# Kernel optimization log

Measured on AMD Instinct MI355X. Metric: run time of the kernel, lower is better.

Reference implementation:

```python
import jax, jax.numpy as jnp
import numpy as np

QMAX = 127.0

def setup_inputs() -> dict:
    key = jax.random.key(0)
    kx, kw, ks = jax.random.split(key, 3)
    B, S, D_IN, D_OUT = 4, 2048, 4096, 4096
    x = jax.random.normal(kx, (B, S, D_IN), dtype=jnp.float16)
    # int8 weight buffer, same distribution as torch.randint(-127, 127)
    weight = jax.random.randint(kw, (D_OUT, D_IN), -127, 127, dtype=jnp.int32).astype(jnp.int8)
    # per-output-channel weight scales (fp16 buffer); small positive values
    weight_scales = (jax.random.uniform(ks, (D_OUT,), dtype=jnp.float32) * 0.01 + 1e-4).astype(jnp.float16)
    return {"x": x, "weight": weight, "weight_scales": weight_scales}

def reference(x, weight, weight_scales):
    # x: [B, S, D_in] fp16; weight: [D_out, D_in] int8; weight_scales: [D_out] fp16
    x32 = x.astype(jnp.float32)
    # dynamic per-token absmax quantization: scale = absmax / 127
    absmax = jnp.max(jnp.abs(x32), axis=-1, keepdims=True)      # [B, S, 1]
    x_scales = jnp.maximum(absmax / QMAX, 1e-8)
    q = jnp.round(x32 / x_scales)                                # in [-127, 127]
    q = jnp.clip(q, -QMAX, QMAX).astype(jnp.int8)
    # int8 GEMM accumulated in int32 (cupy.matmul on int32 in the original)
    y = jnp.einsum('bsk,nk->bsn', q.astype(jnp.int32), weight.astype(jnp.int32),
                   preferred_element_type=jnp.int32)             # [B, S, D_out]
    # dequant: per-token activation scale * per-channel weight scale
    y = y.astype(jnp.float32) * x_scales * weight_scales.astype(jnp.float32)[None, None, :]
    return y.astype(jnp.float16)
```

## Files before the change

kernel.cpp:

```cpp
#include <hip/hip_runtime.h>
#include <stdint.h>

typedef int int32x4 __attribute__((ext_vector_type(4)));

constexpr int K_DIM = 4096;
constexpr int N_DIM = 4096;
constexpr float QMAXF = 127.0f;

__global__ __launch_bounds__(256) void quant_t(const float* __restrict__ x,
                                               int8_t* __restrict__ qt,
                                               float* __restrict__ scales) {
    __shared__ int8_t lq[16][4112];
    const int b = blockIdx.x;
    const int tid = threadIdx.x;
    const int row16 = tid >> 4;
    const int j = tid & 15;
    const size_t rbase = ((size_t)b * 16 + row16) * K_DIM;
    const float4* xr = reinterpret_cast<const float4*>(x + rbase);

    float m = 0.0f;
#pragma unroll 4
    for (int i = 0; i < 16; ++i) {
        const int c = j + 16 * i;
#pragma unroll
        for (int s = 0; s < 4; ++s) {
            float4 v = xr[c * 4 + s];
            m = fmaxf(m, fmaxf(fmaxf(fabsf(v.x), fabsf(v.y)),
                               fmaxf(fabsf(v.z), fabsf(v.w))));
        }
    }
#pragma unroll
    for (int off = 8; off > 0; off >>= 1) m = fmaxf(m, __shfl_xor(m, off));
    const float scale = fmaxf(m * (1.0f / 127.0f), 1e-8f);
    if (j == 0) scales[b * 16 + row16] = scale;
    const float inv = 1.0f / scale;

#pragma unroll 4
    for (int i = 0; i < 16; ++i) {
        const int c = j + 16 * i;
        int w[4];
#pragma unroll
        for (int s = 0; s < 4; ++s) {
            float4 v = xr[c * 4 + s];
            int b0 = ((int)fminf(QMAXF, fmaxf(-QMAXF, rintf(v.x * inv)))) & 255;
            int b1 = ((int)fminf(QMAXF, fmaxf(-QMAXF, rintf(v.y * inv)))) & 255;
            int b2 = ((int)fminf(QMAXF, fmaxf(-QMAXF, rintf(v.z * inv)))) & 255;
            int b3 = ((int)fminf(QMAXF, fmaxf(-QMAXF, rintf(v.w * inv)))) & 255;
            w[s] = b0 | (b1 << 8) | (b2 << 16) | (b3 << 24);
        }
        *reinterpret_cast<int32x4*>(&lq[row16][c * 16]) = (int32x4){w[0], w[1], w[2], w[3]};
    }
    __syncthreads();

    int8_t* outp = qt + (size_t)b * 65536;
#pragma unroll
    for (int i = 0; i < 16; ++i) {
        const int u = tid + 256 * i;
        int32x4 v = *reinterpret_cast<const int32x4*>(&lq[u & 15][(u >> 4) * 16]);
        *reinterpret_cast<int32x4*>(outp + (size_t)u * 16) = v;
    }
}

__global__ __launch_bounds__(256) void pack_w(const int* __restrict__ w,
                                              int8_t* __restrict__ w8) {
    const int idx = blockIdx.x * 256 + threadIdx.x;
    const int4 v = reinterpret_cast<const int4*>(w)[idx];
    int packed = (v.x & 255) | ((v.y & 255) << 8) | ((v.z & 255) << 16) | ((v.w & 255) << 24);
    reinterpret_cast<int*>(w8)[idx] = packed;
}

constexpr int BM = 256, BN = 256, BKB = 128;
constexpr int NT = K_DIM / BKB;
constexpr int BSLOT = 32768;

#define GLL(src, dst)                                                          \
    __builtin_amdgcn_global_load_lds(                                          \
        (const __attribute__((address_space(1))) unsigned int*)(src),          \
        (__attribute__((address_space(3))) unsigned int*)(dst), 16, 0, 0)

#define MFMA_I8(a, b, c) __builtin_amdgcn_mfma_i32_16x16x64_i8((a), (b), (c), 0, 0, 0)

__global__ __launch_bounds__(512, 2) void w8a8_flat(
        const int8_t* __restrict__ QT, const int8_t* __restrict__ B,
        const float* __restrict__ asc, const float* __restrict__ wsc,
        float* __restrict__ C, int M) {
    extern __shared__ int8_t lds[];

    const int tid  = threadIdx.x;
    const int lane = tid & 63;
    const int wave = tid >> 6;

    const int nwg = gridDim.x;
    const int bid = blockIdx.x;
    const int swz = (bid & 7) * (nwg >> 3) + (bid >> 3);
    const int NB  = N_DIM / BN;
    const int brow = (swz / NB) * BM;
    const int bcol = (swz % NB) * BN;

    const int wm = wave & 3;
    const int wn = wave >> 2;
    const int l15 = lane & 15;
    const int ls  = lane >> 4;

    const int8_t* qa = QT + (size_t)(brow >> 4) * 65536 + lane * 16;

    const int rowst = tid >> 3;
    const int gsl   = ((tid & 7) ^ (rowst & 7)) * 16;
    const int8_t* gB = B + (size_t)(bcol + rowst) * K_DIM + gsl;
    const size_t chB = (size_t)64 * K_DIM;
    const int segb = wave * 1024;

    const int boff = (wn * 128 + l15) * BKB + ((ls ^ (l15 & 7)) * 16);

    int32x4 acc[4][8];
#pragma unroll
    for (int i = 0; i < 4; ++i)
#pragma unroll
        for (int j = 0; j < 8; ++j) acc[i][j] = (int32x4){0, 0, 0, 0};

    int32x4 avA[8], avB[8];

#pragma unroll
    for (int mi = 0; mi < 4; ++mi) {
        const int8_t* ap = qa + (((wm * 4 + mi) * 64) << 10);
        avA[2 * mi]     = *(const int32x4*)(ap);
        avA[2 * mi + 1] = *(const int32x4*)(ap + 1024);
    }
#pragma unroll
    for (int c = 0; c < 4; ++c) GLL(gB + c * chB, lds + c * 8192 + segb);
#pragma unroll
    for (int c = 0; c < 4; ++c) GLL(gB + 128 + c * chB, lds + BSLOT + c * 8192 + segb);
    asm volatile("s_waitcnt vmcnt(4)" ::: "memory");
    __builtin_amdgcn_s_barrier();

#define TILE_BODY(T, AVC, AVN)                                                 \
    {                                                                          \
        const int8_t* Bb = lds + ((T) % 3) * BSLOT;                            \
        const bool pf1 = ((T) + 1 < NT);                                       \
        const bool pf2 = ((T) + 2 < NT);                                       \
        int32x4 bf[2][2];                                                      \
        bf[0][0] = *(const int32x4*)(Bb + boff);                               \
        bf[0][1] = *(const int32x4*)(Bb + (boff ^ 64));                        \
        _Pragma("unroll")                                                      \
        for (int ni = 0; ni < 8; ++ni) {                                       \
            const int cur = ni & 1, nxt = cur ^ 1;                             \
            if (ni < 4 && pf1) {                                               \
                const int8_t* ap = qa +                                        \
                    ((((wm * 4 + ni) * 64) + ((T) + 1) * 2) << 10);            \
                AVN[2 * ni]     = *(const int32x4*)(ap);                       \
                AVN[2 * ni + 1] = *(const int32x4*)(ap + 1024);                \
            }                                                                  \
            if (ni == 4 && pf2) {                                              \
                int8_t* dst = lds + (((T) + 2) % 3) * BSLOT;                   \
                _Pragma("unroll")                                              \
                for (int c = 0; c < 4; ++c)                                    \
                    GLL(gB + ((T) + 2) * 128 + c * chB,                        \
                        dst + c * 8192 + segb);                                \
            }                                                                  \
            if (ni < 7) {                                                      \
                const int o = boff + (ni + 1) * 2048;                          \
                bf[nxt][0] = *(const int32x4*)(Bb + o);                        \
                bf[nxt][1] = *(const int32x4*)(Bb + (o ^ 64));                 \
                asm volatile("s_waitcnt lgkmcnt(2)" ::: "memory");             \
            } else {                                                           \
                asm volatile("s_waitcnt lgkmcnt(0)" ::: "memory");             \
            }                                                                  \
            __builtin_amdgcn_sched_barrier(0);                                 \
            __builtin_amdgcn_s_setprio(1);                                     \
            _Pragma("unroll")                                                  \
            for (int mi = 0; mi < 4; ++mi) {                                   \
                acc[mi][ni] = MFMA_I8(AVC[2 * mi], bf[cur][0], acc[mi][ni]);   \
                acc[mi][ni] = MFMA_I8(AVC[2 * mi + 1], bf[cur][1], acc[mi][ni]); \
            }                                                                  \
            __builtin_amdgcn_s_setprio(0);                                     \
        }                                                                      \
        if ((T) < NT - 1) asm volatile("s_waitcnt vmcnt(8)" ::: "memory");     \
        else              asm volatile("s_waitcnt vmcnt(0)" ::: "memory");     \
        __builtin_amdgcn_sched_barrier(0);                                     \
        __builtin_amdgcn_s_barrier();                                          \
    }

    for (int t = 0; t < NT; t += 2) {
        TILE_BODY(t,     avA, avB);
        TILE_BODY(t + 1, avB, avA);
    }

    const int c0  = lane & 15;
    const int rr0 = (lane >> 4) * 4;
#pragma unroll
    for (int ni = 0; ni < 8; ++ni) {
        const int col = bcol + wn * 128 + ni * 16 + c0;
        const float ws = wsc[col];
#pragma unroll
        for (int mi = 0; mi < 4; ++mi) {
            const int rowb = brow + wm * 64 + mi * 16 + rr0;
#pragma unroll
            for (int r = 0; r < 4; ++r) {
                const int row = rowb + r;
                float o = (float)acc[mi][ni][r] * asc[row] * ws;
                o = (float)(_Float16)o;
                C[(size_t)row * N_DIM + col] = o;
            }
        }
    }
}

extern "C" void kernel_launch(void* const* d_in, const int* in_sizes, int n_in,
                              void* d_out, int out_size, void* d_ws, size_t ws_size,
                              hipStream_t stream) {
    const float* x   = (const float*)d_in[0];
    const int*   w   = (const int*)d_in[1];
    const float* wsc = (const float*)d_in[2];
    float* out = (float*)d_out;

    const int K = K_DIM;
    const int M = in_sizes[0] / K;
    const int N = N_DIM;

    int8_t* qt  = (int8_t*)d_ws;
    int8_t* w8  = (int8_t*)d_ws + (size_t)M * K;
    float*  asc = (float*)((char*)d_ws + (size_t)M * K + (size_t)N * K);

    quant_t<<<M / 16, 256, 0, stream>>>(x, qt, asc);
    pack_w<<<(N * (K / 4)) / 256, 256, 0, stream>>>(w, w8);
    const int grid = (M / BM) * (N / BN);
    w8a8_flat<<<grid, 512, 98304, stream>>>(qt, w8, asc, wsc, out, M);
}
```

Baseline: 206.7 us.

## Switch to double-buffered LDS and drop A-register prefetch for higher occupancy

```diff
diff --git a/kernel.cpp b/kernel.cpp
--- a/kernel.cpp
+++ b/kernel.cpp
@@ -80,7 +80,7 @@
 
 #define MFMA_I8(a, b, c) __builtin_amdgcn_mfma_i32_16x16x64_i8((a), (b), (c), 0, 0, 0)
 
-__global__ __launch_bounds__(512, 2) void w8a8_flat(
+__global__ __launch_bounds__(512, 4) void w8a8_flat(
         const int8_t* __restrict__ QT, const int8_t* __restrict__ B,
         const float* __restrict__ asc, const float* __restrict__ wsc,
         float* __restrict__ C, int M) {
@@ -118,71 +118,57 @@
 #pragma unroll
         for (int j = 0; j < 8; ++j) acc[i][j] = (int32x4){0, 0, 0, 0};
 
-    int32x4 avA[8], avB[8];
-
-#pragma unroll
-    for (int mi = 0; mi < 4; ++mi) {
-        const int8_t* ap = qa + (((wm * 4 + mi) * 64) << 10);
-        avA[2 * mi]     = *(const int32x4*)(ap);
-        avA[2 * mi + 1] = *(const int32x4*)(ap + 1024);
-    }
 #pragma unroll
     for (int c = 0; c < 4; ++c) GLL(gB + c * chB, lds + c * 8192 + segb);
-#pragma unroll
-    for (int c = 0; c < 4; ++c) GLL(gB + 128 + c * chB, lds + BSLOT + c * 8192 + segb);
-    asm volatile("s_waitcnt vmcnt(4)" ::: "memory");
+    asm volatile("s_waitcnt vmcnt(0)" ::: "memory");
     __builtin_amdgcn_s_barrier();
 
-#define TILE_BODY(T, AVC, AVN)                                                 \
-    {                                                                          \
-        const int8_t* Bb = lds + ((T) % 3) * BSLOT;                            \
-        const bool pf1 = ((T) + 1 < NT);                                       \
-        const bool pf2 = ((T) + 2 < NT);                                       \
-        int32x4 bf[2][2];                                                      \
-        bf[0][0] = *(const int32x4*)(Bb + boff);                               \
-        bf[0][1] = *(const int32x4*)(Bb + (boff ^ 64));                        \
-        _Pragma("unroll")                                                      \
-        for (int ni = 0; ni < 8; ++ni) {                                       \
-            const int cur = ni & 1, nxt = cur ^ 1;                             \
-            if (ni < 4 && pf1) {                                               \
-                const int8_t* ap = qa +                                        \
-                    ((((wm * 4 + ni) * 64) + ((T) + 1) * 2) << 10);            \
-                AVN[2 * ni]     = *(const int32x4*)(ap);                       \
-                AVN[2 * ni + 1] = *(const int32x4*)(ap + 1024);                \
-            }                                                                  \
-            if (ni == 4 && pf2) {                                              \
-                int8_t* dst = lds + (((T) + 2) % 3) * BSLOT;                   \
-                _Pragma("unroll")                                              \
-                for (int c = 0; c < 4; ++c)                                    \
-                    GLL(gB + ((T) + 2) * 128 + c * chB,                        \
-                        dst + c * 8192 + segb);                                \
-            }                                                                  \
-            if (ni < 7) {                                                      \
-                const int o = boff + (ni + 1) * 2048;                          \
-                bf[nxt][0] = *(const int32x4*)(Bb + o);                        \
-                bf[nxt][1] = *(const int32x4*)(Bb + (o ^ 64));                 \
-                asm volatile("s_waitcnt lgkmcnt(2)" ::: "memory");             \
-            } else {                                                           \
-                asm volatile("s_waitcnt lgkmcnt(0)" ::: "memory");             \
-            }                                                                  \
-            __builtin_amdgcn_sched_barrier(0);                                 \
-            __builtin_amdgcn_s_setprio(1);                                     \
-            _Pragma("unroll")                                                  \
-            for (int mi = 0; mi < 4; ++mi) {                                   \
-                acc[mi][ni] = MFMA_I8(AVC[2 * mi], bf[cur][0], acc[mi][ni]);   \
-                acc[mi][ni] = MFMA_I8(AVC[2 * mi + 1], bf[cur][1], acc[mi][ni]); \
-            }                                                                  \
-            __builtin_amdgcn_s_setprio(0);                                     \
-        }                                                                      \
-        if ((T) < NT - 1) asm volatile("s_waitcnt vmcnt(8)" ::: "memory");     \
-        else              asm volatile("s_waitcnt vmcnt(0)" ::: "memory");     \
-        __builtin_amdgcn_sched_barrier(0);                                     \
-        __builtin_amdgcn_s_barrier();                                          \
-    }
-
-    for (int t = 0; t < NT; t += 2) {
-        TILE_BODY(t,     avA, avB);
-        TILE_BODY(t + 1, avB, avA);
+    int32x4 af[8];
+
+    for (int t = 0; t < NT; ++t) {
+        const int8_t* Bb = lds + (t & 1) * BSLOT;
+        const bool pf = (t + 1 < NT);
+
+#pragma unroll
+        for (int mi = 0; mi < 4; ++mi) {
+            const int8_t* ap = qa + ((((wm * 4 + mi) * 64) + t * 2) << 10);
+            af[2 * mi]     = *(const int32x4*)(ap);
+            af[2 * mi + 1] = *(const int32x4*)(ap + 1024);
+        }
+        if (pf) {
+            int8_t* dst = lds + ((t + 1) & 1) * BSLOT;
+#pragma unroll
+            for (int c = 0; c < 4; ++c)
+                GLL(gB + (t + 1) * 128 + c * chB, dst + c * 8192 + segb);
+        }
+
+        int32x4 bf[2][2];
+        bf[0][0] = *(const int32x4*)(Bb + boff);
+        bf[0][1] = *(const int32x4*)(Bb + (boff ^ 64));
+#pragma unroll
+        for (int ni = 0; ni < 8; ++ni) {
+            const int cur = ni & 1, nxt = cur ^ 1;
+            if (ni < 7) {
+                const int o = boff + (ni + 1) * 2048;
+                bf[nxt][0] = *(const int32x4*)(Bb + o);
+                bf[nxt][1] = *(const int32x4*)(Bb + (o ^ 64));
+                asm volatile("s_waitcnt lgkmcnt(2)" ::: "memory");
+            } else {
+                asm volatile("s_waitcnt lgkmcnt(0)" ::: "memory");
+            }
+            __builtin_amdgcn_sched_barrier(0);
+            __builtin_amdgcn_s_setprio(1);
+#pragma unroll
+            for (int mi = 0; mi < 4; ++mi) {
+                acc[mi][ni] = MFMA_I8(af[2 * mi], bf[cur][0], acc[mi][ni]);
+                acc[mi][ni] = MFMA_I8(af[2 * mi + 1], bf[cur][1], acc[mi][ni]);
+            }
+            __builtin_amdgcn_s_setprio(0);
+        }
+
+        asm volatile("s_waitcnt vmcnt(0)" ::: "memory");
+        __builtin_amdgcn_sched_barrier(0);
+        __builtin_amdgcn_s_barrier();
     }
 
     const int c0  = lane & 15;
@@ -224,5 +210,5 @@
     quant_t<<<M / 16, 256, 0, stream>>>(x, qt, asc);
     pack_w<<<(N * (K / 4)) / 256, 256, 0, stream>>>(w, w8);
     const int grid = (M / BM) * (N / BN);
-    w8a8_flat<<<grid, 512, 98304, stream>>>(qt, w8, asc, wsc, out, M);
-}
+    w8a8_flat<<<grid, 512, 65536, stream>>>(qt, w8, asc, wsc, out, M);
+}
```

Result: slower. 782.4 us (+278.4%).
